# Kernel tuning notes

Hardware: AMD Instinct MI355X
Metric: run time of the kernel (lower is better)

The kernel has to match this reference:

```python
import jax, jax.numpy as jnp
import numpy as np

F = 5            # n_feat = sum(feat_mask)
N_THETAS = 16
N_RHOS = 5
K = N_THETAS * N_RHOS   # 80 Gaussian kernel bins
R = 16           # n_rotations
MAX_RHO = 12.0
S = 1000         # n_samples (patches)
V = 200          # n_vertices per patch
EPS = 1e-5
TWO_PI = 2.0 * np.pi


def _initial_coords():
    # ConvLayer.compute_initial_coordinates: polar grid of (rho, theta) centers
    grid_rho = np.linspace(0.0, MAX_RHO, num=N_RHOS + 1)[1:]
    grid_theta = np.linspace(0.0, TWO_PI, num=N_THETAS + 1)[:-1]
    gr, gt = np.meshgrid(grid_rho, grid_theta)
    return gr.T.flatten().astype(np.float32), gt.T.flatten().astype(np.float32)


def setup_inputs() -> dict:
    key = jax.random.key(0)
    ks = jax.random.split(key, 5)
    feat = jax.random.normal(ks[0], (S, V, F), jnp.float32)
    rho = jax.random.uniform(ks[1], (S, V), jnp.float32) * MAX_RHO
    theta = jax.random.uniform(ks[2], (S, V), jnp.float32) * TWO_PI
    mask = (jax.random.uniform(ks[3], (S, V), jnp.float32) < 0.9).astype(jnp.float32)
    x = jnp.concatenate([feat, rho[..., None], theta[..., None], mask[..., None]], axis=-1)

    gr, gt = _initial_coords()
    mu_rho = jnp.tile(jnp.asarray(gr)[None, :], (F, 1))        # [F, K]
    mu_theta = jnp.tile(jnp.asarray(gt)[None, :], (F, 1))      # [F, K]
    sigma_rho = jnp.full((F, K), MAX_RHO / 8.0, jnp.float32)
    sigma_theta = jnp.ones((F, K), jnp.float32)
    # VarianceScaling(scale=1, fan_avg, uniform): limit = sqrt(3/fan_avg), fan_avg=K
    limit = float(np.sqrt(3.0 / K))
    W_conv = jax.random.uniform(ks[4], (F, K, K), jnp.float32, -limit, limit)
    b_conv = jnp.zeros((F, K), jnp.float32)
    return dict(x=x, mu_rho=mu_rho, sigma_rho=sigma_rho, mu_theta=mu_theta,
                sigma_theta=sigma_theta, W_conv=W_conv, b_conv=b_conv)


def reference(x, mu_rho, sigma_rho, mu_theta, sigma_theta, W_conv, b_conv):
    n_samples = x.shape[0]
    feat = jnp.moveaxis(x[..., :F], -1, 0)          # [F, S, V]
    rho = x[..., 5]                                 # [S, V]
    theta = x[..., 6]                               # [S, V]
    mask = x[..., 7]                                # [S, V]

    inv_sr = 1.0 / (jnp.square(sigma_rho) + EPS)    # [F, K]
    inv_st = 1.0 / (jnp.square(sigma_theta) + EPS)  # [F, K]
    # rho Gaussians are rotation-independent: [F, S, V, K]
    rho_g = jnp.exp(-jnp.square(rho[None, :, :, None] - mu_rho[:, None, None, :])
                    * inv_sr[:, None, None, :])

    def body(carry, k):
        th = jnp.mod(theta + k * (TWO_PI / R), TWO_PI)          # [S, V]
        th_g = jnp.exp(-jnp.square(th[None, :, :, None] - mu_theta[:, None, None, :])
                       * inv_st[:, None, None, :])              # [F, S, V, K]
        act = rho_g * th_g * mask[None, :, :, None]
        act = act / (jnp.sum(act, axis=-1, keepdims=True) + EPS)  # normalize over K bins
        desc = jnp.einsum('fsvk,fsv->fsk', act, feat)           # masked reduce over vertices
        cf = jnp.einsum('fsk,fkj->fsj', desc, W_conv) + b_conv[:, None, :]
        return jnp.maximum(carry, cf), None

    init = jnp.full((F, n_samples, K), -jnp.inf, x.dtype)
    conv, _ = jax.lax.scan(jax.checkpoint(body), init, jnp.arange(R, dtype=x.dtype))
    conv = jax.nn.relu(conv)                        # [F, S, K]
    # tf.stack(ret, axis=2) -> [S, K, F]; reshape [-1, K*F]
    return jnp.transpose(conv, (1, 2, 0)).reshape(n_samples, K * F)
```

## Files before the change

### kernel.cpp

```cpp
#include <hip/hip_runtime.h>
#include <math.h>

#define NS 1000
#define NV 200
#define NF 5
#define NK 80
#define EPSF 1e-5f

#define TWOPI_F 6.28318530717958647692f
#define STEP_F  0.39269908169872414f
#define INV_STEP_F 2.5464790894703254f

#define EH_OFF_H   7424
#define INV2_OFF   6288
#define MSRG_OFF   9872
#define SMEM_FLOATS 10072
#define G_STRIDE_H 232
#define DESC_JSTRIDE 408

typedef __attribute__((ext_vector_type(8))) short short8;
typedef __attribute__((ext_vector_type(4))) float f32x4;

static __device__ __forceinline__ float frcp(float v) {
    return __builtin_amdgcn_rcpf(v);
}
static __device__ __forceinline__ unsigned short f2bf(float x) {
    unsigned u = __float_as_uint(x);
    return (unsigned short)((u + 0x7FFFu + ((u >> 16) & 1u)) >> 16);
}

__global__ __launch_bounds__(512, 8) void lsres_fused(
        const float* __restrict__ x,
        const float* __restrict__ mu_rho,
        const float* __restrict__ sigma_rho,
        const float* __restrict__ mu_theta,
        const float* __restrict__ sigma_theta,
        const float* __restrict__ Wc,
        const float* __restrict__ bc,
        float* __restrict__ out) {
    __shared__ __align__(16) float smem[SMEM_FLOATS];
    unsigned short* smemh = (unsigned short*)smem;

    const int s   = blockIdx.x;
    const int tid = threadIdx.x;

    if (tid < NV) {
        const int v = tid;
        const float* xe = x + ((size_t)s * NV + v) * 8;
        float4 x0 = *(const float4*)(xe);
        float4 x1 = *(const float4*)(xe + 4);
        float rho = x1.y, theta = x1.z, mask = x1.w;
        float fm[5] = {x0.x * mask, x0.y * mask, x0.z * mask, x0.w * mask, x1.x * mask};
        float rg[5];
        float srg = 0.0f;
#pragma unroll
        for (int r = 0; r < 5; ++r) {
            float mr  = mu_rho[r * 16];
            float sr  = sigma_rho[r * 16];
            float isr = 1.0f / (sr * sr + EPSF);
            float d = rho - mr;
            rg[r] = __expf(-d * d * isr);
            srg += rg[r];
        }
#pragma unroll
        for (int f = 0; f < 5; ++f)
#pragma unroll
            for (int r = 0; r < 5; ++r)
                smemh[(f * 5 + r) * G_STRIDE_H + v] = f2bf(fm[f] * rg[r]);

        int m0 = (int)floorf(theta * INV_STEP_F + 0.5f) - 10;
        float sgt = sigma_theta[0];
        float ist = 1.0f / (sgt * sgt + EPSF);
        float m0d = (float)m0 * STEP_F;
#pragma unroll
        for (int cc = 0; cc < 21; ++cc) {
            float mu = fmaf((float)cc, STEP_F, m0d);
            float d  = theta - mu;
            smemh[EH_OFF_H + v * 23 + cc] = f2bf(__expf(-d * d * ist));
        }
        smem[MSRG_OFF + v] = mask * srg;
    } else if (tid < 224) {
        const int v = tid;
#pragma unroll
        for (int cc = 0; cc < 23; ++cc) smemh[EH_OFF_H + v * 23 + cc] = 0;
#pragma unroll
        for (int m = 0; m < 32; ++m) smemh[m * G_STRIDE_H + v] = 0;
    } else if (tid < 256) {
        for (int i = tid - 224; i < 7 * G_STRIDE_H; i += 32)
            smemh[25 * G_STRIDE_H + i] = 0;
    }
    __syncthreads();

#pragma unroll
    for (int p = 0; p < 7; ++p) {
        int idx = tid + p * 512;
        int v  = idx >> 4;
        int jj = idx & 15;
        unsigned bits;
        if (v < NV) {
            float theta = x[((size_t)s * NV + v) * 8 + 6];
            float msrg  = smem[MSRG_OFF + v];
            int   m0 = (int)floorf(theta * INV_STEP_F + 0.5f) - 10;
            float th = theta + (float)jj * STEP_F;
            int b = ((th >= TWOPI_F) ? 16 : 0) - jj - m0;
            float sT = 0.0f;
#pragma unroll
            for (int t = 0; t < 16; ++t) {
                int ic = min(max(b + t, 0), 20);
                sT += __uint_as_float((unsigned)smemh[EH_OFF_H + v * 23 + ic] << 16);
            }
            float inv = frcp(fmaf(msrg, sT, EPSF));
            bits = (__float_as_uint(inv) & 0xFFFFFF00u) | (unsigned)(b + 128);
        } else {
            bits = 128u;
        }
        smem[INV2_OFF + idx] = __uint_as_float(bits);
    }
    __syncthreads();

    const int lane = tid & 63;
    const int wv   = tid >> 6;
    const int ln   = lane & 15;
    const int g    = lane >> 4;
    const int j0   = wv * 2, j1 = j0 + 1;

    f32x4 c00 = {0.f, 0.f, 0.f, 0.f};
    f32x4 c01 = {0.f, 0.f, 0.f, 0.f};
    f32x4 c10 = {0.f, 0.f, 0.f, 0.f};
    f32x4 c11 = {0.f, 0.f, 0.f, 0.f};
    const char* smemb = (const char*)smem;
    const int abase = ln * 464 + g * 16;

#pragma unroll 1
    for (int kb = 0; kb < 7; ++kb) {
        short8 a0 = *(const short8*)(smemb + abase + kb * 64);
        short8 a1 = *(const short8*)(smemb + abase + 7424 + kb * 64);
        const int vb = kb * 32 + g * 8;

        union Frag { unsigned u[4]; short8 v8; } B0, B1;
#define BUILD_B(DST, J)                                                              \
        {                                                                            \
            _Pragma("unroll")                                                        \
            for (int p = 0; p < 4; ++p) {                                            \
                float pb0 = smem[INV2_OFF + ((vb + 2 * p) << 4) + (J)];              \
                float pb1 = smem[INV2_OFF + ((vb + 2 * p + 1) << 4) + (J)];          \
                int ic0 = min(max(ln + (int)(__float_as_uint(pb0) & 255u) - 128, 0), 20); \
                int ic1 = min(max(ln + (int)(__float_as_uint(pb1) & 255u) - 128, 0), 20); \
                float e0 = __uint_as_float((unsigned)smemh[EH_OFF_H + (vb + 2 * p) * 23 + ic0] << 16); \
                float e1 = __uint_as_float((unsigned)smemh[EH_OFF_H + (vb + 2 * p + 1) * 23 + ic1] << 16); \
                float act0 = e0 * pb0;                                               \
                float act1 = e1 * pb1;                                               \
                asm("v_cvt_pk_bf16_f32 %0, %1, %2" : "=v"(DST.u[p]) : "v"(act0), "v"(act1)); \
            }                                                                        \
        }
        BUILD_B(B0, j0)
        BUILD_B(B1, j1)
#undef BUILD_B
        c00 = __builtin_amdgcn_mfma_f32_16x16x32_bf16(a0, B0.v8, c00, 0, 0, 0);
        c10 = __builtin_amdgcn_mfma_f32_16x16x32_bf16(a1, B0.v8, c10, 0, 0, 0);
        c01 = __builtin_amdgcn_mfma_f32_16x16x32_bf16(a0, B1.v8, c01, 0, 0, 0);
        c11 = __builtin_amdgcn_mfma_f32_16x16x32_bf16(a1, B1.v8, c11, 0, 0, 0);
    }
    __syncthreads();

#pragma unroll
    for (int q = 0; q < 4; ++q) {
        int m  = g * 4 + q;
        int f  = (m * 13) >> 6;
        int r  = m - 5 * f;
        int o  = f * 80 + r * 16 + ln;
        smem[j0 * DESC_JSTRIDE + o] = c00[q];
        smem[j1 * DESC_JSTRIDE + o] = c01[q];
        int m2 = 16 + g * 4 + q;
        if (m2 < 25) {
            int f2 = (m2 * 13) >> 6;
            int r2 = m2 - 5 * f2;
            int o2 = f2 * 80 + r2 * 16 + ln;
            smem[j0 * DESC_JSTRIDE + o2] = c10[q];
            smem[j1 * DESC_JSTRIDE + o2] = c11[q];
        }
    }
    __syncthreads();

    if (tid < 400) {
        const float4* smem4v = (const float4*)smem;
        const int f    = tid / 80;
        const int rem  = tid % 80;
        const int pair = rem >> 1;
        const int jh   = rem & 1;
        const int jo   = pair * 2;

        float a2[8][2];
#pragma unroll
        for (int i = 0; i < 8; ++i) { a2[i][0] = 0.0f; a2[i][1] = 0.0f; }

        const float* Wf = Wc + f * (NK * NK);
        for (int k4 = 0; k4 < 20; ++k4) {
            const float* wp = Wf + (k4 * 4) * NK + jo;
            float2 w0 = *(const float2*)(wp);
            float2 w1 = *(const float2*)(wp + NK);
            float2 w2 = *(const float2*)(wp + 2 * NK);
            float2 w3 = *(const float2*)(wp + 3 * NK);
#pragma unroll
            for (int i = 0; i < 8; ++i) {
                int jj = jh * 8 + i;
                float4 d4 = smem4v[jj * 102 + f * 20 + k4];
                a2[i][0] = fmaf(d4.x, w0.x, a2[i][0]);
                a2[i][0] = fmaf(d4.y, w1.x, a2[i][0]);
                a2[i][0] = fmaf(d4.z, w2.x, a2[i][0]);
                a2[i][0] = fmaf(d4.w, w3.x, a2[i][0]);
                a2[i][1] = fmaf(d4.x, w0.y, a2[i][1]);
                a2[i][1] = fmaf(d4.y, w1.y, a2[i][1]);
                a2[i][1] = fmaf(d4.z, w2.y, a2[i][1]);
                a2[i][1] = fmaf(d4.w, w3.y, a2[i][1]);
            }
        }

        float m0v = -INFINITY, m1v = -INFINITY;
#pragma unroll
        for (int i = 0; i < 8; ++i) {
            m0v = fmaxf(m0v, a2[i][0]);
            m1v = fmaxf(m1v, a2[i][1]);
        }
        m0v = fmaxf(m0v, __shfl_xor(m0v, 1));
        m1v = fmaxf(m1v, __shfl_xor(m1v, 1));

        float mv  = jh ? m1v : m0v;
        float val = fmaxf(mv + bc[f * NK + jo + jh], 0.0f);
        out[(size_t)s * (NK * NF) + (jo + jh) * NF + f] = val;
    }
}

extern "C" void kernel_launch(void* const* d_in, const int* in_sizes, int n_in,
                              void* d_out, int out_size, void* d_ws, size_t ws_size,
                              hipStream_t stream) {
    const float* x           = (const float*)d_in[0];
    const float* mu_rho      = (const float*)d_in[1];
    const float* sigma_rho   = (const float*)d_in[2];
    const float* mu_theta    = (const float*)d_in[3];
    const float* sigma_theta = (const float*)d_in[4];
    const float* Wc          = (const float*)d_in[5];
    const float* bc          = (const float*)d_in[6];
    float* out = (float*)d_out;

    lsres_fused<<<dim3(NS), dim3(512), 0, stream>>>(
        x, mu_rho, sigma_rho, mu_theta, sigma_theta, Wc, bc, out);
}
```

Measured before the change: 109.7 us.

## Use bf16 MFMA for the W_conv projection and transpose the normalizer table

The per-rotation projection of descriptors through W_conv now runs as 16x16x32 bf16 MFMAs spread across all 8 waves. It replaces the scalar fp32 FMA loop that only used 400 threads. Descriptors are stored in shared memory as bf16 with zero padding for the K dimension, and weights are converted to bf16 on the fly. The inverse-normalizer table is also laid out jj-major with an odd stride to reduce LDS bank conflicts when building B fragments. Rounding descriptors and weights to bf16 loses some precision in the output.

```diff
diff --git a/kernel.cpp b/kernel.cpp
--- a/kernel.cpp
+++ b/kernel.cpp
@@ -11,12 +11,13 @@
 #define STEP_F  0.39269908169872414f
 #define INV_STEP_F 2.5464790894703254f
 
-#define EH_OFF_H   7424
-#define INV2_OFF   6288
-#define MSRG_OFF   9872
-#define SMEM_FLOATS 10072
-#define G_STRIDE_H 232
-#define DESC_JSTRIDE 408
+#define EH_OFF_H    7424
+#define INV2_OFF    6288
+#define INV2_STRIDE 225
+#define MSRG_OFF    9888
+#define SMEM_FLOATS 10088
+#define G_STRIDE_H  232
+#define DESC_STRIDE_H 488
 
 typedef __attribute__((ext_vector_type(8))) short short8;
 typedef __attribute__((ext_vector_type(4))) float f32x4;
@@ -92,29 +93,31 @@
     __syncthreads();
 
 #pragma unroll
-    for (int p = 0; p < 7; ++p) {
+    for (int p = 0; p < 8; ++p) {
         int idx = tid + p * 512;
-        int v  = idx >> 4;
-        int jj = idx & 15;
-        unsigned bits;
-        if (v < NV) {
-            float theta = x[((size_t)s * NV + v) * 8 + 6];
-            float msrg  = smem[MSRG_OFF + v];
-            int   m0 = (int)floorf(theta * INV_STEP_F + 0.5f) - 10;
-            float th = theta + (float)jj * STEP_F;
-            int b = ((th >= TWOPI_F) ? 16 : 0) - jj - m0;
-            float sT = 0.0f;
-#pragma unroll
-            for (int t = 0; t < 16; ++t) {
-                int ic = min(max(b + t, 0), 20);
-                sT += __uint_as_float((unsigned)smemh[EH_OFF_H + v * 23 + ic] << 16);
+        if (idx < 3600) {
+            int v  = idx >> 4;
+            int jj = idx & 15;
+            unsigned bits;
+            if (v < NV) {
+                float theta = x[((size_t)s * NV + v) * 8 + 6];
+                float msrg  = smem[MSRG_OFF + v];
+                int   m0 = (int)floorf(theta * INV_STEP_F + 0.5f) - 10;
+                float th = theta + (float)jj * STEP_F;
+                int b = ((th >= TWOPI_F) ? 16 : 0) - jj - m0;
+                float sT = 0.0f;
+#pragma unroll
+                for (int t = 0; t < 16; ++t) {
+                    int ic = min(max(b + t, 0), 20);
+                    sT += __uint_as_float((unsigned)smemh[EH_OFF_H + v * 23 + ic] << 16);
+                }
+                float inv = frcp(fmaf(msrg, sT, EPSF));
+                bits = (__float_as_uint(inv) & 0xFFFFFF00u) | (unsigned)(b + 128);
+            } else {
+                bits = 128u;
             }
-            float inv = frcp(fmaf(msrg, sT, EPSF));
-            bits = (__float_as_uint(inv) & 0xFFFFFF00u) | (unsigned)(b + 128);
-        } else {
-            bits = 128u;
-        }
-        smem[INV2_OFF + idx] = __uint_as_float(bits);
+            smem[INV2_OFF + jj * INV2_STRIDE + v] = __uint_as_float(bits);
+        }
     }
     __syncthreads();
 
@@ -142,8 +145,8 @@
         {                                                                            \
             _Pragma("unroll")                                                        \
             for (int p = 0; p < 4; ++p) {                                            \
-                float pb0 = smem[INV2_OFF + ((vb + 2 * p) << 4) + (J)];              \
-                float pb1 = smem[INV2_OFF + ((vb + 2 * p + 1) << 4) + (J)];          \
+                float pb0 = smem[INV2_OFF + (J) * INV2_STRIDE + (vb + 2 * p)];       \
+                float pb1 = smem[INV2_OFF + (J) * INV2_STRIDE + (vb + 2 * p + 1)];   \
                 int ic0 = min(max(ln + (int)(__float_as_uint(pb0) & 255u) - 128, 0), 20); \
                 int ic1 = min(max(ln + (int)(__float_as_uint(pb1) & 255u) - 128, 0), 20); \
                 float e0 = __uint_as_float((unsigned)smemh[EH_OFF_H + (vb + 2 * p) * 23 + ic0] << 16); \
@@ -163,71 +166,66 @@
     }
     __syncthreads();
 
-#pragma unroll
-    for (int q = 0; q < 4; ++q) {
-        int m  = g * 4 + q;
-        int f  = (m * 13) >> 6;
-        int r  = m - 5 * f;
-        int o  = f * 80 + r * 16 + ln;
-        smem[j0 * DESC_JSTRIDE + o] = c00[q];
-        smem[j1 * DESC_JSTRIDE + o] = c01[q];
-        int m2 = 16 + g * 4 + q;
-        if (m2 < 25) {
-            int f2 = (m2 * 13) >> 6;
-            int r2 = m2 - 5 * f2;
-            int o2 = f2 * 80 + r2 * 16 + ln;
-            smem[j0 * DESC_JSTRIDE + o2] = c10[q];
-            smem[j1 * DESC_JSTRIDE + o2] = c11[q];
-        }
-    }
-    __syncthreads();
-
-    if (tid < 400) {
-        const float4* smem4v = (const float4*)smem;
-        const int f    = tid / 80;
-        const int rem  = tid % 80;
-        const int pair = rem >> 1;
-        const int jh   = rem & 1;
-        const int jo   = pair * 2;
-
-        float a2[8][2];
-#pragma unroll
-        for (int i = 0; i < 8; ++i) { a2[i][0] = 0.0f; a2[i][1] = 0.0f; }
-
-        const float* Wf = Wc + f * (NK * NK);
-        for (int k4 = 0; k4 < 20; ++k4) {
-            const float* wp = Wf + (k4 * 4) * NK + jo;
-            float2 w0 = *(const float2*)(wp);
-            float2 w1 = *(const float2*)(wp + NK);
-            float2 w2 = *(const float2*)(wp + 2 * NK);
-            float2 w3 = *(const float2*)(wp + 3 * NK);
-#pragma unroll
-            for (int i = 0; i < 8; ++i) {
-                int jj = jh * 8 + i;
-                float4 d4 = smem4v[jj * 102 + f * 20 + k4];
-                a2[i][0] = fmaf(d4.x, w0.x, a2[i][0]);
-                a2[i][0] = fmaf(d4.y, w1.x, a2[i][0]);
-                a2[i][0] = fmaf(d4.z, w2.x, a2[i][0]);
-                a2[i][0] = fmaf(d4.w, w3.x, a2[i][0]);
-                a2[i][1] = fmaf(d4.x, w0.y, a2[i][1]);
-                a2[i][1] = fmaf(d4.y, w1.y, a2[i][1]);
-                a2[i][1] = fmaf(d4.z, w2.y, a2[i][1]);
-                a2[i][1] = fmaf(d4.w, w3.y, a2[i][1]);
+    {
+#pragma unroll
+        for (int q = 0; q < 4; ++q) {
+            int m = g * 4 + q;
+            int f = (m * 13) >> 6;
+            int r = m - 5 * f;
+            int o = f * 96 + r * 16 + ln;
+            unsigned pk;
+            asm("v_cvt_pk_bf16_f32 %0, %1, %2" : "=v"(pk) : "v"(c00[q]), "v"(c01[q]));
+            smemh[j0 * DESC_STRIDE_H + o] = (unsigned short)pk;
+            smemh[j1 * DESC_STRIDE_H + o] = (unsigned short)(pk >> 16);
+            int m2 = 16 + m;
+            if (m2 < 25) {
+                int f2 = (m2 * 13) >> 6;
+                int r2 = m2 - 5 * f2;
+                int o2 = f2 * 96 + r2 * 16 + ln;
+                unsigned pk2;
+                asm("v_cvt_pk_bf16_f32 %0, %1, %2" : "=v"(pk2) : "v"(c10[q]), "v"(c11[q]));
+                smemh[j0 * DESC_STRIDE_H + o2] = (unsigned short)pk2;
+                smemh[j1 * DESC_STRIDE_H + o2] = (unsigned short)(pk2 >> 16);
             }
         }
-
-        float m0v = -INFINITY, m1v = -INFINITY;
-#pragma unroll
-        for (int i = 0; i < 8; ++i) {
-            m0v = fmaxf(m0v, a2[i][0]);
-            m1v = fmaxf(m1v, a2[i][1]);
-        }
-        m0v = fmaxf(m0v, __shfl_xor(m0v, 1));
-        m1v = fmaxf(m1v, __shfl_xor(m1v, 1));
-
-        float mv  = jh ? m1v : m0v;
-        float val = fmaxf(mv + bc[f * NK + jo + jh], 0.0f);
-        out[(size_t)s * (NK * NF) + (jo + jh) * NF + f] = val;
+        unsigned* d32 = (unsigned*)smem;
+        for (int i = tid; i < 640; i += 512) {
+            int jj = i / 40;
+            int rm = i - jj * 40;
+            int ff = rm >> 3;
+            int w  = rm & 7;
+            d32[jj * 244 + ff * 48 + 40 + w] = 0;
+        }
+    }
+    __syncthreads();
+
+    for (int job = wv; job < 25; job += 8) {
+        const int f  = job / 5;
+        const int nt = job - f * 5;
+        const float* Wf = Wc + f * (NK * NK) + nt * 16 + ln;
+
+        f32x4 cc = {0.f, 0.f, 0.f, 0.f};
+#pragma unroll
+        for (int kb = 0; kb < 3; ++kb) {
+            short8 afr = *(const short8*)((const char*)smem
+                          + ln * 976 + (f * 96 + kb * 32 + g * 8) * 2);
+            union { unsigned u[4]; short8 v8; } bfr;
+#pragma unroll
+            for (int p = 0; p < 4; ++p) {
+                int k0 = kb * 32 + g * 8 + 2 * p;
+                float w0 = Wf[min(k0, 79) * NK];
+                float w1 = Wf[min(k0 + 1, 79) * NK];
+                asm("v_cvt_pk_bf16_f32 %0, %1, %2" : "=v"(bfr.u[p]) : "v"(w0), "v"(w1));
+            }
+            cc = __builtin_amdgcn_mfma_f32_16x16x32_bf16(afr, bfr.v8, cc, 0, 0, 0);
+        }
+        float m = fmaxf(fmaxf(cc[0], cc[1]), fmaxf(cc[2], cc[3]));
+        m = fmaxf(m, __shfl_xor(m, 16));
+        m = fmaxf(m, __shfl_xor(m, 32));
+        if (g == 0) {
+            float val = fmaxf(m + bc[f * NK + nt * 16 + ln], 0.0f);
+            out[(size_t)s * (NK * NF) + (nt * 16 + ln) * NF + f] = val;
+        }
     }
 }
 
```

Result: faster. 98.57 us (-10.1%).
